# Optimization experiments

Measured on AMD Instinct MI355X. Metric: run time of the kernel, lower is better.

Reference implementation:

```python
import jax, jax.numpy as jnp
import numpy as np

_LOG_2PI = float(np.log(2.0 * np.pi))
N = 4096
N_VARS = 128
N_SOURCES = 8
_EPS = 1e-6


def setup_inputs() -> dict:
    key = jax.random.key(0)
    ks = jax.random.split(key, 6)
    data = jax.random.normal(ks[0], (N, N_VARS), dtype=jnp.float32)
    sources = jax.random.randint(ks[1], (N,), 0, N_SOURCES, dtype=jnp.int32)
    miss_mask = jax.random.bernoulli(ks[2], 0.3, (N, N_VARS))
    # Strictly lower-triangular DAG weights, small spectral norm so I - W is well conditioned
    W_eff = jnp.tril(jax.random.normal(ks[3], (N_VARS, N_VARS), dtype=jnp.float32) * 0.05, k=-1)
    log_sigma2 = jnp.zeros((N_SOURCES, N_VARS), dtype=jnp.float32)
    mu = jnp.zeros((N_VARS,), dtype=jnp.float32)
    sample_weights = jax.random.uniform(ks[4], (N,), dtype=jnp.float32)
    return {"data": data, "W_eff": W_eff, "log_sigma2": log_sigma2, "mu": mu,
            "sample_weights": sample_weights, "sources": sources, "miss_mask": miss_mask}


def reference(data, W_eff, log_sigma2, mu, sample_weights, sources, miss_mask):
    # Gaussian log-likelihood over observed entries only, per sample.
    # Original torch code loops over unique (source, missingness-pattern) groups and
    # does a Cholesky of the observed sub-covariance Sigma_oo + eps*I.  We compute the
    # mathematically identical quantity fully batched via the masked-covariance trick:
    #   Sigma_tilde = M (Sigma + eps I) M + diag(1 - obs)
    # whose logdet equals logdet(Sigma_oo + eps I_oo) and whose quadratic form on the
    # zero-filled centred data equals x_o^T (Sigma_oo + eps I)^{-1} x_o.
    D = data.shape[1]
    I = jnp.eye(D, dtype=data.dtype)
    T = jnp.linalg.solve(I - W_eff, I)                       # [D, D]
    sigma2 = jnp.maximum(jnp.exp(log_sigma2), _EPS)          # [S, D]
    # Sigma_s = T^T diag(sigma2_s) T for every source
    Sigma = jnp.einsum('ij,si,ik->sjk', T, sigma2, T)        # [S, D, D]

    obs = (~miss_mask).astype(data.dtype)                    # [N, D]
    xc = (data - mu[None, :]) * obs                          # centred, zero at missing

    Sig_i = Sigma[sources] + _EPS * I                        # [N, D, D]
    M = obs[:, :, None] * obs[:, None, :]                    # [N, D, D] obs outer obs
    Sig_t = Sig_i * M + I * (1.0 - obs)[:, None, :]          # identity on missing coords

    L = jnp.linalg.cholesky(Sig_t)                           # [N, D, D]
    z = jax.scipy.linalg.solve_triangular(L, xc[:, :, None], lower=True)[:, :, 0]
    quad = jnp.sum(z * z, axis=1)                            # [N]
    logdet = 2.0 * jnp.sum(jnp.log(jnp.diagonal(L, axis1=1, axis2=2)), axis=1)
    d_obs = jnp.sum(obs, axis=1)                             # [N]
    ll = -0.5 * (quad + logdet + d_obs * _LOG_2PI)           # [N]
    return jnp.sum(ll * sample_weights)
```

## Files before the change

### kernel.cpp

```cpp
#include <hip/hip_runtime.h>
#include <math.h>

#define DD 128
#define NSRC 8
#define EMAX 32
#define MFAST 62
#define LOG_2PI 1.83787706640934548356f
#define LN2F 0.69314718055994531f
#define EPSF 1e-6f

__device__ inline int tri_row_of(int e) {
    float f = sqrtf(8.f * (float)e + 1.f);
    int r = (int)((f - 1.f) * 0.5f);
    if ((r + 1) * (r + 2) / 2 <= e) ++r;
    else if (r * (r + 1) / 2 > e) --r;
    return r;
}

__global__ __launch_bounds__(128) void k_precompute(
    const float* __restrict__ W, const float* __restrict__ ls2,
    const unsigned int* __restrict__ mw, int n_words,
    float* __restrict__ Q, float* __restrict__ ldS, int* __restrict__ flag)
{
    __shared__ float Bs[DD][DD + 1];
    __shared__ float r[4][DD + 1];
    __shared__ float sinv[DD];
    __shared__ float part2[2];
    const int tid = threadIdx.x;
    const int s   = blockIdx.x >> 5;
    const int i0  = (blockIdx.x & 31) * 4;

    int gid = (blockIdx.x * 128 + tid) * 4;
    int f = 0;
    #pragma unroll
    for (int t = 0; t < 4; ++t) {
        int idx = gid + t;
        if (idx < n_words) {
            unsigned int v = mw[idx];
            if (v > 1u) f |= 1;
            if (v == 0x3F800000u) f |= 2;
        }
    }
    unsigned long long bA = __ballot(f & 1);
    unsigned long long bB = __ballot(f & 2);
    if ((tid & 63) == 0) {
        int fw = (bA ? 1 : 0) | (bB ? 2 : 0);
        if (fw) atomicOr(flag, fw);
    }

    for (int idx = tid; idx < DD * DD; idx += 128) {
        int row = idx >> 7, col = idx & 127;
        Bs[row][col] = (row == col ? 1.f : 0.f) - W[idx];
    }
    sinv[tid] = 1.f / fmaxf(expf(ls2[s * DD + tid]), EPSF);
    __syncthreads();
    for (int a = 0; a < 4; ++a)
        r[a][tid] = Bs[i0 + a][tid] * sinv[tid];
    __syncthreads();

    const int j = tid;
    float acc0 = 0.f, acc1 = 0.f, acc2 = 0.f, acc3 = 0.f;
    #pragma unroll 4
    for (int d = 0; d < DD; ++d) {
        float bj = Bs[j][d];
        acc0 += r[0][d] * bj;
        acc1 += r[1][d] * bj;
        acc2 += r[2][d] * bj;
        acc3 += r[3][d] * bj;
    }
    size_t base = ((size_t)s * DD + i0) * DD + j;
    Q[base         ] = acc0;
    Q[base +     DD] = acc1;
    Q[base + 2 * DD] = acc2;
    Q[base + 3 * DD] = acc3;

    if (i0 == 0) {
        float v = logf(fmaxf(expf(ls2[s * DD + tid]), EPSF));
        for (int o = 32; o; o >>= 1) v += __shfl_down(v, o, 64);
        if ((tid & 63) == 0) part2[tid >> 6] = v;
        __syncthreads();
        if (tid == 0) ldS[s] = part2[0] + part2[1];
    }
}

__global__ __launch_bounds__(64) void k_fast(
    const float* __restrict__ data, const float* __restrict__ mu,
    const float* __restrict__ wgt, const int* __restrict__ src,
    const void* __restrict__ miss, const int* __restrict__ layoutFlag,
    const float* __restrict__ Q, const float* __restrict__ ldS,
    float* __restrict__ partial, int* __restrict__ ovf_count,
    int* __restrict__ ovf_list)
{
    __shared__ float xsh[DD];
    __shared__ float ysh[DD];
    __shared__ int   midx[64];
    __shared__ float csc[2][64];
    __shared__ float tri[(MFAST + 1) * (MFAST + 2) / 2];

    const int i = blockIdx.x, lane = threadIdx.x;
    const int s = src[i];
    const float* Qs = Q + (size_t)s * DD * DD;
    const size_t base = (size_t)i * DD;
    const int j0 = 2 * lane, j1 = 2 * lane + 1;

    const int f = *layoutFlag;
    bool mmE, mmO;
    if (f & 2) {
        const float* M = (const float*)miss;
        mmE = M[base + j0] != 0.f;  mmO = M[base + j1] != 0.f;
    } else if (f & 1) {
        const unsigned char* M = (const unsigned char*)miss;
        mmE = M[base + j0] != 0;    mmO = M[base + j1] != 0;
    } else {
        const int* M = (const int*)miss;
        mmE = M[base + j0] != 0;    mmO = M[base + j1] != 0;
    }

    unsigned long long bE = __ballot(mmE), bO = __ballot(mmO);
    const int m = __popcll(bE) + __popcll(bO);
    if (m > MFAST) {
        if (lane == 0) { int pos = atomicAdd(ovf_count, 1); ovf_list[pos] = i; }
        return;
    }
    unsigned long long lt = (1ull << lane) - 1ull;
    if (mmE) midx[__popcll(bE & lt)] = j0;
    if (mmO) midx[__popcll(bE) + __popcll(bO & lt)] = j1;

    float x0 = mmE ? 0.f : (data[base + j0] - mu[j0]);
    float x1 = mmO ? 0.f : (data[base + j1] - mu[j1]);
    xsh[j0] = x0;
    xsh[j1] = x1;
    __syncthreads();

    float y0 = 0.f, y1 = 0.f;
    #pragma unroll 4
    for (int k = 0; k < DD; ++k) {
        float xk = xsh[k];
        if (xk != 0.f) {
            float2 q = *(const float2*)(Qs + (size_t)k * DD + j0);
            y0 += xk * q.x;
            y1 += xk * q.y;
        }
    }
    ysh[j0] = y0;
    ysh[j1] = y1;
    float p = x0 * y0 + x1 * y1;
    for (int o = 32; o; o >>= 1) p += __shfl_down(p, o, 64);
    __syncthreads();

    const int mjc = midx[lane];
    for (int ir = 0; ir < m; ++ir) {
        int row = midx[ir];
        if (lane <= ir)
            tri[((ir * (ir + 1)) >> 1) + lane] = Qs[(size_t)row * DD + mjc];
    }
    const int offm = (m * (m + 1)) >> 1;
    if (lane < m)   tri[offm + lane] = ysh[mjc];
    if (lane == 0)  tri[offm + m] = 0.f;
    __syncthreads();

    const int cntT = ((m + 1) * (m + 2)) >> 1;
    unsigned key[EMAX];
    float    val[EMAX];
    #pragma unroll
    for (int t = 0; t < EMAX; ++t) {
        key[t] = 0u; val[t] = 0.f;
        int e = lane + (t << 6);
        if (e < cntT) {
            int q  = tri_row_of(e);
            int jc = m - q;
            int ir = jc + (e - ((q * (q + 1)) >> 1));
            float v = tri[((ir * (ir + 1)) >> 1) + jc];
            key[t] = ((unsigned)jc << 8) | (unsigned)ir;
            val[t] = v;
            if (jc == 0) csc[0][ir] = v;
        }
    }
    __syncthreads();

    float logacc = 0.f;
    #pragma unroll 1
    for (int k = 0; k < m; ++k) {
        const int pb = k & 1;
        float dk = csc[pb][k];
        float invd = __builtin_amdgcn_rcpf(dk);
        logacc += __log2f(dk);
        const unsigned boundA = (unsigned)(k + 1) << 8;
        const unsigned boundB = (unsigned)(k + 2) << 8;
        #pragma unroll
        for (int t = 0; t < EMAX; ++t) {
            bool alive = (key[t] >= boundA);
            if (!__any(alive)) break;
            if (alive) {
                int ir = (int)(key[t] & 255u);
                int jc = (int)(key[t] >> 8);
                float ci = csc[pb][ir];
                float cj = csc[pb][jc];
                val[t] -= ci * cj * invd;
                if (key[t] < boundB) csc[pb ^ 1][ir] = val[t];
            }
        }
        __syncthreads();
    }

    if (lane == 0) {
        float ll = -0.5f * ((p + val[0]) + logacc * LN2F + ldS[s]
                            + (float)(DD - m) * LOG_2PI);
        atomicAdd(&partial[i & 63], ll * wgt[i]);
    }
}

__global__ __launch_bounds__(128) void k_tail(
    const float* __restrict__ data, const float* __restrict__ mu,
    const float* __restrict__ wgt, const int* __restrict__ src,
    const void* __restrict__ miss, const int* __restrict__ layoutFlag,
    const float* __restrict__ Q, const float* __restrict__ ldS,
    float* __restrict__ partial, const int* __restrict__ ovf_count,
    const int* __restrict__ ovf_list, float* __restrict__ out)
{
    __shared__ __align__(16) float xsh[DD];
    __shared__ float ysh[DD];
    __shared__ int   midx[DD];
    __shared__ float cscv[DD + 1];
    __shared__ float tri[(DD + 1) * (DD + 2) / 2];
    __shared__ float bc[2];
    __shared__ float red[2];
    __shared__ int   sh_m;

    const int tid = threadIdx.x;
    const int novf = *ovf_count;
    for (int j = 0; j < novf; ++j) {
        const int i = ovf_list[j];
        if (tid == 0) sh_m = 0;
        __syncthreads();

        const int s = src[i];
        const float* Qs = Q + (size_t)s * DD * DD;
        const int f = *layoutFlag;
        const size_t g = (size_t)i * DD + tid;
        bool mm;
        if (f & 2)      mm = ((const float*)miss)[g] != 0.f;
        else if (f & 1) mm = ((const unsigned char*)miss)[g] != 0;
        else            mm = ((const int*)miss)[g] != 0;

        float xv = mm ? 0.f : (data[g] - mu[tid]);
        xsh[tid] = xv;
        if (mm) { int pos = atomicAdd(&sh_m, 1); midx[pos] = tid; }
        __syncthreads();
        const int m = sh_m;

        const float4* qrow = (const float4*)(Qs + (size_t)tid * DD);
        const float4* x4   = (const float4*)xsh;
        float acc = 0.f;
        #pragma unroll 8
        for (int d = 0; d < DD / 4; ++d) {
            float4 q = qrow[d], xx = x4[d];
            acc += q.x * xx.x + q.y * xx.y + q.z * xx.z + q.w * xx.w;
        }
        ysh[tid] = acc;
        float pp = xv * acc;
        for (int o = 32; o; o >>= 1) pp += __shfl_down(pp, o, 64);
        if ((tid & 63) == 0) red[tid >> 6] = pp;
        __syncthreads();

        const int cntA = (m * (m + 1)) >> 1;
        for (int e = tid; e < cntA; e += 128) {
            int a = tri_row_of(e);
            int b = e - ((a * (a + 1)) >> 1);
            tri[e] = Qs[(size_t)midx[a] * DD + midx[b]];
        }
        for (int b = tid; b < m; b += 128) tri[cntA + b] = ysh[midx[b]];
        if (tid == 0) tri[cntA + m] = 0.f;
        __syncthreads();

        float logacc = 0.f;
        if (m > 0) {
            if (tid == 0) {
                float d0 = tri[0];
                bc[1] = d0;
                float sq = sqrtf(d0);
                bc[0] = 1.f / sq;
                tri[0] = sq;
            }
            __syncthreads();
            for (int k = 0; k < m; ++k) {
                float inv = bc[0];
                if (tid == 0) logacc += logf(bc[1]);
                for (int ii = k + 1 + tid; ii <= m; ii += 128) {
                    int off = (ii * (ii + 1)) >> 1;
                    float v = tri[off + k] * inv;
                    tri[off + k] = v;
                    cscv[ii] = v;
                }
                __syncthreads();
                int qn  = m - k;
                int cnt = (qn * (qn + 1)) >> 1;
                for (int e = tid; e < cnt; e += 128) {
                    int ri = tri_row_of(e);
                    int rj = e - ((ri * (ri + 1)) >> 1);
                    int ii = k + 1 + ri, jj = k + 1 + rj;
                    int off = (ii * (ii + 1)) >> 1;
                    float v = tri[off + jj] - cscv[ii] * cscv[jj];
                    if (ii == jj && jj == k + 1 && k + 1 < m) {
                        bc[1] = v;
                        float sq = sqrtf(v);
                        bc[0] = 1.f / sq;
                        tri[off + jj] = sq;
                    } else {
                        tri[off + jj] = v;
                    }
                }
                __syncthreads();
            }
        }

        if (tid == 0) {
            float quad2 = (m > 0) ? -tri[cntA + m] : 0.f;
            float quad1 = red[0] + red[1];
            float ll = -0.5f * ((quad1 - quad2) + logacc + ldS[s]
                                + (float)(DD - m) * LOG_2PI);
            atomicAdd(&partial[i & 63], ll * wgt[i]);
        }
        __syncthreads();
    }

    __syncthreads();
    if (tid < 64) {
        float v = partial[tid];
        for (int o = 32; o; o >>= 1) v += __shfl_down(v, o, 64);
        if (tid == 0) out[0] = v;
    }
}

extern "C" void kernel_launch(void* const* d_in, const int* in_sizes, int n_in,
                              void* d_out, int out_size, void* d_ws, size_t ws_size,
                              hipStream_t stream)
{
    const float* data = (const float*)d_in[0];
    const float* W    = (const float*)d_in[1];
    const float* ls2  = (const float*)d_in[2];
    const float* mu   = (const float*)d_in[3];
    const float* wgt  = (const float*)d_in[4];
    const int*   src  = (const int*)d_in[5];
    const void*  miss = (const void*)d_in[6];
    float* out = (float*)d_out;

    float* Q        = (float*)d_ws;
    float* ldS      = Q + (size_t)NSRC * DD * DD;
    float* partial  = ldS + NSRC;
    int*   flag     = (int*)(partial + 64);
    int*   ovf_cnt  = flag + 1;
    int*   ovf_list = flag + 2;

    const int n       = in_sizes[0] / DD;
    const int n_words = (n * DD) / 4;

    hipMemsetAsync(partial, 0, 66 * sizeof(float), stream);
    hipLaunchKernelGGL(k_precompute, dim3(NSRC * 32), dim3(128), 0, stream,
                       W, ls2, (const unsigned int*)miss, n_words, Q, ldS, flag);
    hipLaunchKernelGGL(k_fast, dim3(n), dim3(64), 0, stream,
                       data, mu, wgt, src, miss, flag, Q, ldS,
                       partial, ovf_cnt, ovf_list);
    hipLaunchKernelGGL(k_tail, dim3(1), dim3(128), 0, stream,
                       data, mu, wgt, src, miss, flag, Q, ldS,
                       partial, ovf_cnt, ovf_list, out);
}
```

Measured before the change: 162.4 us.

## Fold memset and tail kernel into precompute and last-block reduction

Removes the hipMemsetAsync and the separate k_tail launch. Zeroing of counters now happens inside k_precompute, and the layout flag goes to a per-block array instead of an atomic. k_fast elects its last block with a done counter, and that block handles overflow samples serially in one thread and writes the final reduction. The matrix-vector loop is also unrolled with two accumulators and the xk!=0 skip is dropped. The goal is to cut launch and memset overhead, at the cost of a very slow single-thread path whenever overflow samples exist.

```diff
diff --git a/kernel.cpp b/kernel.cpp
--- a/kernel.cpp
+++ b/kernel.cpp
@@ -20,7 +20,9 @@
 __global__ __launch_bounds__(128) void k_precompute(
     const float* __restrict__ W, const float* __restrict__ ls2,
     const unsigned int* __restrict__ mw, int n_words,
-    float* __restrict__ Q, float* __restrict__ ldS, int* __restrict__ flag)
+    float* __restrict__ Q, float* __restrict__ ldS,
+    int* __restrict__ flagarr, float* __restrict__ partial,
+    int* __restrict__ ovf_cnt, int* __restrict__ done_cnt)
 {
     __shared__ float Bs[DD][DD + 1];
     __shared__ float r[4][DD + 1];
@@ -29,6 +31,12 @@
     const int tid = threadIdx.x;
     const int s   = blockIdx.x >> 5;
     const int i0  = (blockIdx.x & 31) * 4;
+
+    if (blockIdx.x == 0) {
+        if (tid < 64)  partial[tid] = 0.f;
+        if (tid == 64) *ovf_cnt = 0;
+        if (tid == 65) *done_cnt = 0;
+    }
 
     int gid = (blockIdx.x * 128 + tid) * 4;
     int f = 0;
@@ -43,10 +51,8 @@
     }
     unsigned long long bA = __ballot(f & 1);
     unsigned long long bB = __ballot(f & 2);
-    if ((tid & 63) == 0) {
-        int fw = (bA ? 1 : 0) | (bB ? 2 : 0);
-        if (fw) atomicOr(flag, fw);
-    }
+    __shared__ int fsh[2];
+    if ((tid & 63) == 0) fsh[tid >> 6] = (bA ? 1 : 0) | (bB ? 2 : 0);
 
     for (int idx = tid; idx < DD * DD; idx += 128) {
         int row = idx >> 7, col = idx & 127;
@@ -54,6 +60,7 @@
     }
     sinv[tid] = 1.f / fmaxf(expf(ls2[s * DD + tid]), EPSF);
     __syncthreads();
+    if (tid == 0) flagarr[blockIdx.x] = fsh[0] | fsh[1];
     for (int a = 0; a < 4; ++a)
         r[a][tid] = Bs[i0 + a][tid] * sinv[tid];
     __syncthreads();
@@ -86,10 +93,11 @@
 __global__ __launch_bounds__(64) void k_fast(
     const float* __restrict__ data, const float* __restrict__ mu,
     const float* __restrict__ wgt, const int* __restrict__ src,
-    const void* __restrict__ miss, const int* __restrict__ layoutFlag,
+    const void* __restrict__ miss, const int* __restrict__ flagarr,
     const float* __restrict__ Q, const float* __restrict__ ldS,
-    float* __restrict__ partial, int* __restrict__ ovf_count,
-    int* __restrict__ ovf_list)
+    float* __restrict__ partial, int* __restrict__ ovf_cnt,
+    int* __restrict__ done_cnt, int* __restrict__ ovf_list,
+    float* __restrict__ scratch, float* __restrict__ out)
 {
     __shared__ float xsh[DD];
     __shared__ float ysh[DD];
@@ -103,7 +111,13 @@
     const size_t base = (size_t)i * DD;
     const int j0 = 2 * lane, j1 = 2 * lane + 1;
 
-    const int f = *layoutFlag;
+    int fl = 0;
+    #pragma unroll
+    for (int t = 0; t < 4; ++t) fl |= flagarr[lane + 64 * t];
+    unsigned long long fb1 = __ballot(fl & 1);
+    unsigned long long fb2 = __ballot(fl & 2);
+    const int f = (fb1 ? 1 : 0) | (fb2 ? 2 : 0);
+
     bool mmE, mmO;
     if (f & 2) {
         const float* M = (const float*)miss;
@@ -118,218 +132,166 @@
 
     unsigned long long bE = __ballot(mmE), bO = __ballot(mmO);
     const int m = __popcll(bE) + __popcll(bO);
-    if (m > MFAST) {
-        if (lane == 0) { int pos = atomicAdd(ovf_count, 1); ovf_list[pos] = i; }
-        return;
-    }
-    unsigned long long lt = (1ull << lane) - 1ull;
-    if (mmE) midx[__popcll(bE & lt)] = j0;
-    if (mmO) midx[__popcll(bE) + __popcll(bO & lt)] = j1;
-
-    float x0 = mmE ? 0.f : (data[base + j0] - mu[j0]);
-    float x1 = mmO ? 0.f : (data[base + j1] - mu[j1]);
-    xsh[j0] = x0;
-    xsh[j1] = x1;
-    __syncthreads();
-
-    float y0 = 0.f, y1 = 0.f;
-    #pragma unroll 4
-    for (int k = 0; k < DD; ++k) {
-        float xk = xsh[k];
-        if (xk != 0.f) {
-            float2 q = *(const float2*)(Qs + (size_t)k * DD + j0);
-            y0 += xk * q.x;
-            y1 += xk * q.y;
-        }
-    }
-    ysh[j0] = y0;
-    ysh[j1] = y1;
-    float p = x0 * y0 + x1 * y1;
-    for (int o = 32; o; o >>= 1) p += __shfl_down(p, o, 64);
-    __syncthreads();
-
-    const int mjc = midx[lane];
-    for (int ir = 0; ir < m; ++ir) {
-        int row = midx[ir];
-        if (lane <= ir)
-            tri[((ir * (ir + 1)) >> 1) + lane] = Qs[(size_t)row * DD + mjc];
-    }
-    const int offm = (m * (m + 1)) >> 1;
-    if (lane < m)   tri[offm + lane] = ysh[mjc];
-    if (lane == 0)  tri[offm + m] = 0.f;
-    __syncthreads();
-
-    const int cntT = ((m + 1) * (m + 2)) >> 1;
-    unsigned key[EMAX];
-    float    val[EMAX];
-    #pragma unroll
-    for (int t = 0; t < EMAX; ++t) {
-        key[t] = 0u; val[t] = 0.f;
-        int e = lane + (t << 6);
-        if (e < cntT) {
-            int q  = tri_row_of(e);
-            int jc = m - q;
-            int ir = jc + (e - ((q * (q + 1)) >> 1));
-            float v = tri[((ir * (ir + 1)) >> 1) + jc];
-            key[t] = ((unsigned)jc << 8) | (unsigned)ir;
-            val[t] = v;
-            if (jc == 0) csc[0][ir] = v;
-        }
-    }
-    __syncthreads();
-
-    float logacc = 0.f;
-    #pragma unroll 1
-    for (int k = 0; k < m; ++k) {
-        const int pb = k & 1;
-        float dk = csc[pb][k];
-        float invd = __builtin_amdgcn_rcpf(dk);
-        logacc += __log2f(dk);
-        const unsigned boundA = (unsigned)(k + 1) << 8;
-        const unsigned boundB = (unsigned)(k + 2) << 8;
+    const bool skip = (m > MFAST);
+    if (skip) {
+        if (lane == 0) { int pos = atomicAdd(ovf_cnt, 1); ovf_list[pos] = i; }
+    } else {
+        unsigned long long lt = (1ull << lane) - 1ull;
+        if (mmE) midx[__popcll(bE & lt)] = j0;
+        if (mmO) midx[__popcll(bE) + __popcll(bO & lt)] = j1;
+
+        float x0 = mmE ? 0.f : (data[base + j0] - mu[j0]);
+        float x1 = mmO ? 0.f : (data[base + j1] - mu[j1]);
+        xsh[j0] = x0;
+        xsh[j1] = x1;
+        __syncthreads();
+
+        float y0 = 0.f, y1 = 0.f, z0 = 0.f, z1 = 0.f;
+        #pragma unroll 8
+        for (int k = 0; k < DD; k += 2) {
+            float xk0 = xsh[k], xk1 = xsh[k + 1];
+            float2 qa = *(const float2*)(Qs + (size_t)k * DD + j0);
+            float2 qb = *(const float2*)(Qs + (size_t)(k + 1) * DD + j0);
+            y0 += xk0 * qa.x;  y1 += xk0 * qa.y;
+            z0 += xk1 * qb.x;  z1 += xk1 * qb.y;
+        }
+        y0 += z0;  y1 += z1;
+        ysh[j0] = y0;
+        ysh[j1] = y1;
+        float p = x0 * y0 + x1 * y1;
+        for (int o = 32; o; o >>= 1) p += __shfl_down(p, o, 64);
+        __syncthreads();
+
+        const int mjc = midx[lane];
+        for (int ir = 0; ir < m; ++ir) {
+            int row = midx[ir];
+            if (lane <= ir)
+                tri[((ir * (ir + 1)) >> 1) + lane] = Qs[(size_t)row * DD + mjc];
+        }
+        const int offm = (m * (m + 1)) >> 1;
+        if (lane < m)   tri[offm + lane] = ysh[mjc];
+        if (lane == 0)  tri[offm + m] = 0.f;
+        __syncthreads();
+
+        const int cntT = ((m + 1) * (m + 2)) >> 1;
+        unsigned key[EMAX];
+        float    val[EMAX];
         #pragma unroll
         for (int t = 0; t < EMAX; ++t) {
-            bool alive = (key[t] >= boundA);
-            if (!__any(alive)) break;
-            if (alive) {
-                int ir = (int)(key[t] & 255u);
-                int jc = (int)(key[t] >> 8);
-                float ci = csc[pb][ir];
-                float cj = csc[pb][jc];
-                val[t] -= ci * cj * invd;
-                if (key[t] < boundB) csc[pb ^ 1][ir] = val[t];
-            }
-        }
-        __syncthreads();
-    }
-
-    if (lane == 0) {
-        float ll = -0.5f * ((p + val[0]) + logacc * LN2F + ldS[s]
-                            + (float)(DD - m) * LOG_2PI);
-        atomicAdd(&partial[i & 63], ll * wgt[i]);
-    }
-}
-
-__global__ __launch_bounds__(128) void k_tail(
-    const float* __restrict__ data, const float* __restrict__ mu,
-    const float* __restrict__ wgt, const int* __restrict__ src,
-    const void* __restrict__ miss, const int* __restrict__ layoutFlag,
-    const float* __restrict__ Q, const float* __restrict__ ldS,
-    float* __restrict__ partial, const int* __restrict__ ovf_count,
-    const int* __restrict__ ovf_list, float* __restrict__ out)
-{
-    __shared__ __align__(16) float xsh[DD];
-    __shared__ float ysh[DD];
-    __shared__ int   midx[DD];
-    __shared__ float cscv[DD + 1];
-    __shared__ float tri[(DD + 1) * (DD + 2) / 2];
-    __shared__ float bc[2];
-    __shared__ float red[2];
-    __shared__ int   sh_m;
-
-    const int tid = threadIdx.x;
-    const int novf = *ovf_count;
-    for (int j = 0; j < novf; ++j) {
-        const int i = ovf_list[j];
-        if (tid == 0) sh_m = 0;
-        __syncthreads();
-
-        const int s = src[i];
-        const float* Qs = Q + (size_t)s * DD * DD;
-        const int f = *layoutFlag;
-        const size_t g = (size_t)i * DD + tid;
-        bool mm;
-        if (f & 2)      mm = ((const float*)miss)[g] != 0.f;
-        else if (f & 1) mm = ((const unsigned char*)miss)[g] != 0;
-        else            mm = ((const int*)miss)[g] != 0;
-
-        float xv = mm ? 0.f : (data[g] - mu[tid]);
-        xsh[tid] = xv;
-        if (mm) { int pos = atomicAdd(&sh_m, 1); midx[pos] = tid; }
-        __syncthreads();
-        const int m = sh_m;
-
-        const float4* qrow = (const float4*)(Qs + (size_t)tid * DD);
-        const float4* x4   = (const float4*)xsh;
-        float acc = 0.f;
-        #pragma unroll 8
-        for (int d = 0; d < DD / 4; ++d) {
-            float4 q = qrow[d], xx = x4[d];
-            acc += q.x * xx.x + q.y * xx.y + q.z * xx.z + q.w * xx.w;
-        }
-        ysh[tid] = acc;
-        float pp = xv * acc;
-        for (int o = 32; o; o >>= 1) pp += __shfl_down(pp, o, 64);
-        if ((tid & 63) == 0) red[tid >> 6] = pp;
-        __syncthreads();
-
-        const int cntA = (m * (m + 1)) >> 1;
-        for (int e = tid; e < cntA; e += 128) {
-            int a = tri_row_of(e);
-            int b = e - ((a * (a + 1)) >> 1);
-            tri[e] = Qs[(size_t)midx[a] * DD + midx[b]];
-        }
-        for (int b = tid; b < m; b += 128) tri[cntA + b] = ysh[midx[b]];
-        if (tid == 0) tri[cntA + m] = 0.f;
+            key[t] = 0u; val[t] = 0.f;
+            int e = lane + (t << 6);
+            if (e < cntT) {
+                int q  = tri_row_of(e);
+                int jc = m - q;
+                int ir = jc + (e - ((q * (q + 1)) >> 1));
+                float v = tri[((ir * (ir + 1)) >> 1) + jc];
+                key[t] = ((unsigned)jc << 8) | (unsigned)ir;
+                val[t] = v;
+                if (jc == 0) csc[0][ir] = v;
+            }
+        }
         __syncthreads();
 
         float logacc = 0.f;
-        if (m > 0) {
-            if (tid == 0) {
-                float d0 = tri[0];
-                bc[1] = d0;
-                float sq = sqrtf(d0);
-                bc[0] = 1.f / sq;
-                tri[0] = sq;
+        #pragma unroll 1
+        for (int k = 0; k < m; ++k) {
+            const int pb = k & 1;
+            float dk = csc[pb][k];
+            float invd = __builtin_amdgcn_rcpf(dk);
+            logacc += __log2f(dk);
+            const unsigned boundA = (unsigned)(k + 1) << 8;
+            const unsigned boundB = (unsigned)(k + 2) << 8;
+            #pragma unroll
+            for (int t = 0; t < EMAX; ++t) {
+                bool alive = (key[t] >= boundA);
+                if (!__any(alive)) break;
+                if (alive) {
+                    int ir = (int)(key[t] & 255u);
+                    int jc = (int)(key[t] >> 8);
+                    float ci = csc[pb][ir];
+                    float cj = csc[pb][jc];
+                    val[t] -= ci * cj * invd;
+                    if (key[t] < boundB) csc[pb ^ 1][ir] = val[t];
+                }
             }
             __syncthreads();
-            for (int k = 0; k < m; ++k) {
-                float inv = bc[0];
-                if (tid == 0) logacc += logf(bc[1]);
-                for (int ii = k + 1 + tid; ii <= m; ii += 128) {
-                    int off = (ii * (ii + 1)) >> 1;
-                    float v = tri[off + k] * inv;
-                    tri[off + k] = v;
-                    cscv[ii] = v;
-                }
-                __syncthreads();
-                int qn  = m - k;
-                int cnt = (qn * (qn + 1)) >> 1;
-                for (int e = tid; e < cnt; e += 128) {
-                    int ri = tri_row_of(e);
-                    int rj = e - ((ri * (ri + 1)) >> 1);
-                    int ii = k + 1 + ri, jj = k + 1 + rj;
-                    int off = (ii * (ii + 1)) >> 1;
-                    float v = tri[off + jj] - cscv[ii] * cscv[jj];
-                    if (ii == jj && jj == k + 1 && k + 1 < m) {
-                        bc[1] = v;
-                        float sq = sqrtf(v);
-                        bc[0] = 1.f / sq;
-                        tri[off + jj] = sq;
-                    } else {
-                        tri[off + jj] = v;
-                    }
-                }
-                __syncthreads();
-            }
-        }
-
-        if (tid == 0) {
-            float quad2 = (m > 0) ? -tri[cntA + m] : 0.f;
-            float quad1 = red[0] + red[1];
-            float ll = -0.5f * ((quad1 - quad2) + logacc + ldS[s]
+        }
+
+        if (lane == 0) {
+            float ll = -0.5f * ((p + val[0]) + logacc * LN2F + ldS[s]
                                 + (float)(DD - m) * LOG_2PI);
             atomicAdd(&partial[i & 63], ll * wgt[i]);
         }
-        __syncthreads();
-    }
-
-    __syncthreads();
-    if (tid < 64) {
-        float v = partial[tid];
-        for (int o = 32; o; o >>= 1) v += __shfl_down(v, o, 64);
-        if (tid == 0) out[0] = v;
-    }
+    }
+
+    __threadfence();
+    int ticket = 0;
+    if (lane == 0) ticket = atomicAdd(done_cnt, 1);
+    ticket = __shfl(ticket, 0, 64);
+    if (ticket != (int)gridDim.x - 1) return;
+    __threadfence();
+
+    float extra = 0.f;
+    if (lane == 0) {
+        int novf = atomicAdd(ovf_cnt, 0);
+        float* s_tri = scratch;
+        float* s_xc  = scratch + 8400;
+        int*   s_mi  = (int*)(scratch + 8544);
+        for (int jj = 0; jj < novf; ++jj) {
+            int ii = atomicAdd(&ovf_list[jj], 0);
+            int s2 = src[ii];
+            const float* Q2 = Q + (size_t)s2 * DD * DD;
+            int m2 = 0;
+            for (int d = 0; d < DD; ++d) {
+                size_t g = (size_t)ii * DD + d;
+                bool mm;
+                if (f & 2)      mm = ((const float*)miss)[g] != 0.f;
+                else if (f & 1) mm = ((const unsigned char*)miss)[g] != 0;
+                else            mm = ((const int*)miss)[g] != 0;
+                float xv = mm ? 0.f : (data[g] - mu[d]);
+                s_xc[d] = xv;
+                if (mm) s_mi[m2++] = d;
+            }
+            float quad1 = 0.f;
+            for (int rr = 0; rr < DD; ++rr) {
+                float xr = s_xc[rr];
+                if (xr != 0.f) {
+                    float acc = 0.f;
+                    for (int c = 0; c < DD; ++c) acc += Q2[(size_t)rr * DD + c] * s_xc[c];
+                    quad1 += xr * acc;
+                }
+            }
+            int offm2 = (m2 * (m2 + 1)) >> 1;
+            for (int a = 0; a < m2; ++a) {
+                int ra = s_mi[a];
+                float acc = 0.f;
+                for (int c = 0; c < DD; ++c) acc += Q2[(size_t)ra * DD + c] * s_xc[c];
+                s_tri[offm2 + a] = acc;
+                for (int b = 0; b <= a; ++b)
+                    s_tri[((a * (a + 1)) >> 1) + b] = Q2[(size_t)ra * DD + s_mi[b]];
+            }
+            s_tri[offm2 + m2] = 0.f;
+            float logacc2 = 0.f;
+            for (int k = 0; k < m2; ++k) {
+                float dk = s_tri[((k * (k + 1)) >> 1) + k];
+                logacc2 += logf(dk);
+                float inv = 1.f / dk;
+                for (int a = k + 1; a <= m2; ++a) {
+                    float cik = s_tri[((a * (a + 1)) >> 1) + k];
+                    for (int b = k + 1; b <= a; ++b)
+                        s_tri[((a * (a + 1)) >> 1) + b] -=
+                            cik * s_tri[((b * (b + 1)) >> 1) + k] * inv;
+                }
+            }
+            float ll = -0.5f * ((quad1 + s_tri[offm2 + m2]) + logacc2 + ldS[s2]
+                                + (float)(DD - m2) * LOG_2PI);
+            extra += ll * wgt[ii];
+        }
+    }
+
+    float v = atomicAdd(&partial[lane], 0.f);
+    for (int o = 32; o; o >>= 1) v += __shfl_down(v, o, 64);
+    if (lane == 0) out[0] = v + extra;
 }
 
 extern "C" void kernel_launch(void* const* d_in, const int* in_sizes, int n_in,
@@ -348,20 +310,19 @@
     float* Q        = (float*)d_ws;
     float* ldS      = Q + (size_t)NSRC * DD * DD;
     float* partial  = ldS + NSRC;
-    int*   flag     = (int*)(partial + 64);
-    int*   ovf_cnt  = flag + 1;
-    int*   ovf_list = flag + 2;
+    int*   flagarr  = (int*)(partial + 64);
+    int*   ovf_cnt  = flagarr + 256;
+    int*   done_cnt = ovf_cnt + 1;
+    int*   ovf_list = done_cnt + 1;
+    float* scratch  = (float*)(ovf_list + 4096);
 
     const int n       = in_sizes[0] / DD;
     const int n_words = (n * DD) / 4;
 
-    hipMemsetAsync(partial, 0, 66 * sizeof(float), stream);
     hipLaunchKernelGGL(k_precompute, dim3(NSRC * 32), dim3(128), 0, stream,
-                       W, ls2, (const unsigned int*)miss, n_words, Q, ldS, flag);
+                       W, ls2, (const unsigned int*)miss, n_words,
+                       Q, ldS, flagarr, partial, ovf_cnt, done_cnt);
     hipLaunchKernelGGL(k_fast, dim3(n), dim3(64), 0, stream,
-                       data, mu, wgt, src, miss, flag, Q, ldS,
-                       partial, ovf_cnt, ovf_list);
-    hipLaunchKernelGGL(k_tail, dim3(1), dim3(128), 0, stream,
-                       data, mu, wgt, src, miss, flag, Q, ldS,
-                       partial, ovf_cnt, ovf_list, out);
+                       data, mu, wgt, src, miss, flagarr, Q, ldS,
+                       partial, ovf_cnt, done_cnt, ovf_list, scratch, out);
 }
```

New measurement: 176.5 us. 1.09x slower.
